# Kernel tuning notes

Hardware: AMD Instinct MI355X
Metric: run time of the kernel (lower is better)

Reference implementation:

```python
import jax, jax.numpy as jnp
import numpy as np

B, S, D = 64, 2048, 512

def setup_inputs() -> dict:
    key = jax.random.key(0)
    k1, k2, k3, k4, k5, k6 = jax.random.split(key, 6)
    hidden2 = jax.random.normal(k1, (B, D), dtype=jnp.float32)
    enc_key = jax.random.normal(k2, (B, S, D), dtype=jnp.float32)
    enc_value = jax.random.normal(k3, (B, S, D), dtype=jnp.float32)
    seq_lens = jax.random.randint(k4, (B,), 1, S + 1)  # valid lengths in [1, S]
    W = jax.random.normal(k5, (D, D), dtype=jnp.float32) / np.sqrt(D)
    b = jax.random.normal(k6, (D,), dtype=jnp.float32) * 0.01
    return {"hidden2": hidden2, "key": enc_key, "value": enc_value,
            "seq_lens": seq_lens, "W": W, "b": b}

def reference(hidden2, key, value, seq_lens, W, b):
    # query = Linear(hidden2): [B, D]
    query = hidden2 @ W.T + b
    # scores E = bmm(key, query): [B, S]
    E = jnp.einsum('bsd,bd->bs', key, query)
    # per-sample padding mask: positions >= seq_lens[i] get -inf
    mask = jnp.arange(S)[None, :] < seq_lens[:, None]  # [B, S]
    E = jnp.where(mask, E, -jnp.inf)
    attn = jax.nn.softmax(E, axis=-1)  # [B, S]
    context = jnp.einsum('bs,bsd->bd', attn, value)  # [B, D]
    return (context, attn[:, None, :])  # attn reshaped to [B, 1, S] as in torch
```

## Files before the change

### kernel.cpp

```cpp
#include <hip/hip_runtime.h>
#include <math.h>

#define BB 64
#define SS 2048
#define DD 512
#define SC 64
#define NC (SS / SC)

__global__ void query_kernel(const float* __restrict__ hidden2,
                             const float* __restrict__ W,
                             const float* __restrict__ bias,
                             float* __restrict__ q) {
    const int b    = blockIdx.y;
    const int wave = threadIdx.x >> 6;
    const int lane = threadIdx.x & 63;
    const int d    = blockIdx.x * 4 + wave;

    const float4* h4 = reinterpret_cast<const float4*>(hidden2 + (size_t)b * DD);
    const float4* w4 = reinterpret_cast<const float4*>(W + (size_t)d * DD);
    float4 a0 = h4[lane];
    float4 a1 = h4[64 + lane];
    float4 b0 = w4[lane];
    float4 b1 = w4[64 + lane];
    float p = a0.x*b0.x + a0.y*b0.y + a0.z*b0.z + a0.w*b0.w
            + a1.x*b1.x + a1.y*b1.y + a1.z*b1.z + a1.w*b1.w;
    #pragma unroll
    for (int off = 32; off; off >>= 1) p += __shfl_xor(p, off, 64);
    if (lane == 0) q[b * DD + d] = p + bias[d];
}

__global__ void chunk_kernel(const float* __restrict__ key,
                             const float* __restrict__ value,
                             const float* __restrict__ q,
                             const int* __restrict__ seq_lens,
                             float* __restrict__ attn,
                             float* __restrict__ mc,
                             float* __restrict__ lc,
                             float* __restrict__ ctxp) {
    const int b     = blockIdx.y;
    const int chunk = blockIdx.x;
    const int len   = seq_lens[b];
    const int s0    = chunk * SC;
    if (s0 >= len) return;
    const int nv = min(SC, len - s0);

    const int t    = threadIdx.x;
    const int wave = t >> 6;
    const int lane = t & 63;

    __shared__ float E_lds[SC];
    __shared__ float p_lds[SC];
    __shared__ float red[256];
    __shared__ float4 cred[128];

    const float4* q4 = reinterpret_cast<const float4*>(q + (size_t)b * DD);
    const float4 q0 = q4[lane];
    const float4 q1 = q4[64 + lane];

    for (int r = wave; r < nv; r += 4) {
        const float4* k4 =
            reinterpret_cast<const float4*>(key + ((size_t)b * SS + s0 + r) * DD);
        float4 k0 = k4[lane];
        float4 k1 = k4[64 + lane];
        float p = k0.x*q0.x + k0.y*q0.y + k0.z*q0.z + k0.w*q0.w
                + k1.x*q1.x + k1.y*q1.y + k1.z*q1.z + k1.w*q1.w;
        #pragma unroll
        for (int off = 32; off; off >>= 1) p += __shfl_xor(p, off, 64);
        if (lane == 0) E_lds[r] = p;
    }
    __syncthreads();

    red[t] = (t < nv) ? E_lds[t] : -INFINITY;
    __syncthreads();
    #pragma unroll
    for (int off = 128; off; off >>= 1) {
        if (t < off) red[t] = fmaxf(red[t], red[t + off]);
        __syncthreads();
    }
    const float m_c = red[0];
    __syncthreads();

    float pv = 0.f;
    if (t < nv) {
        pv = __expf(E_lds[t] - m_c);
        p_lds[t] = pv;
        attn[(size_t)b * SS + s0 + t] = pv;
    }
    red[t] = pv;
    __syncthreads();
    #pragma unroll
    for (int off = 128; off; off >>= 1) {
        if (t < off) red[t] += red[t + off];
        __syncthreads();
    }
    if (t == 0) {
        mc[b * NC + chunk] = m_c;
        lc[b * NC + chunk] = red[0];
    }

    const int d4   = t & 127;
    const int half = t >> 7;
    float4 acc = make_float4(0.f, 0.f, 0.f, 0.f);
    for (int r = half; r < nv; r += 2) {
        const float4 v = *reinterpret_cast<const float4*>(
            value + ((size_t)b * SS + s0 + r) * DD + 4 * d4);
        const float p = p_lds[r];
        acc.x += p * v.x; acc.y += p * v.y; acc.z += p * v.z; acc.w += p * v.w;
    }
    __syncthreads();
    if (half) cred[d4] = acc;
    __syncthreads();
    if (!half) {
        const float4 o = cred[d4];
        acc.x += o.x; acc.y += o.y; acc.z += o.z; acc.w += o.w;
        *reinterpret_cast<float4*>(ctxp + ((size_t)b * NC + chunk) * DD + 4 * d4) = acc;
    }
}

__global__ void combine_kernel(const float* __restrict__ mc,
                               const float* __restrict__ lc,
                               const float* __restrict__ ctxp,
                               const int* __restrict__ seq_lens,
                               float* __restrict__ attn,
                               float* __restrict__ ctx) {
    const int b   = blockIdx.x;
    const int t   = threadIdx.x;
    const int len = seq_lens[b];
    const int ncb = (len + SC - 1) / SC;

    __shared__ float sm[2];
    __shared__ float sa[NC];
    __shared__ float sc_[NC];

    if (t < 64) {
        const int lane = t;
        float m_c = (lane < ncb) ? mc[b * NC + lane] : -INFINITY;
        float l_c = (lane < ncb) ? lc[b * NC + lane] : 0.f;
        float m = m_c;
        #pragma unroll
        for (int off = 32; off; off >>= 1) m = fmaxf(m, __shfl_xor(m, off, 64));
        float le = l_c * __expf(m_c - m);
        float l = le;
        #pragma unroll
        for (int off = 32; off; off >>= 1) l += __shfl_xor(l, off, 64);
        if (lane == 0) { sm[0] = m; sm[1] = l; }
        if (lane < NC) {
            float e = (lane < ncb) ? __expf(m_c - m) : 0.f;
            sc_[lane] = e;
            sa[lane]  = e / l;
        }
    }
    __syncthreads();
    const float inv_l = 1.0f / sm[1];

    if (t < 128) {
        float4 acc = make_float4(0.f, 0.f, 0.f, 0.f);
        for (int c = 0; c < ncb; ++c) {
            const float4 v = *reinterpret_cast<const float4*>(
                ctxp + ((size_t)b * NC + c) * DD + 4 * t);
            const float s = sc_[c];
            acc.x += s * v.x; acc.y += s * v.y; acc.z += s * v.z; acc.w += s * v.w;
        }
        acc.x *= inv_l; acc.y *= inv_l; acc.z *= inv_l; acc.w *= inv_l;
        *reinterpret_cast<float4*>(ctx + (size_t)b * DD + 4 * t) = acc;
    }

    float* a = attn + (size_t)b * SS;
    for (int s = t; s < SS; s += 256) {
        if (s < len) a[s] *= sa[s >> 6];
        else         a[s]  = 0.f;
    }
}

extern "C" void kernel_launch(void* const* d_in, const int* in_sizes, int n_in,
                              void* d_out, int out_size, void* d_ws, size_t ws_size,
                              hipStream_t stream) {
    const float* hidden2  = (const float*)d_in[0];
    const float* key      = (const float*)d_in[1];
    const float* value    = (const float*)d_in[2];
    const int*   seq_lens = (const int*)  d_in[3];
    const float* W        = (const float*)d_in[4];
    const float* bias     = (const float*)d_in[5];

    float* out  = (float*)d_out;
    float* ctx  = out;
    float* attn = out + BB * DD;

    float* ws   = (float*)d_ws;
    float* q    = ws;
    float* mc   = ws + BB * DD;
    float* lc   = mc + BB * NC;
    float* ctxp = lc + BB * NC;

    query_kernel  <<<dim3(DD / 4, BB), 256, 0, stream>>>(hidden2, W, bias, q);
    chunk_kernel  <<<dim3(NC, BB),     256, 0, stream>>>(key, value, q, seq_lens,
                                                         attn, mc, lc, ctxp);
    combine_kernel<<<BB,               256, 0, stream>>>(mc, lc, ctxp, seq_lens,
                                                         attn, ctx);
}
```

Baseline: 491.5 us.

## Halve chunk size and replace LDS tree reductions with wave shuffles

Chunk size drops from 64 to 32 rows, doubling the number of chunk blocks to raise parallelism across the GPU. The block-wide max/sum reductions through shared memory with many barriers become a single-wave shuffle reduction, which is possible because a chunk now fits in one wave. The combine kernel is adjusted for 64 chunks per batch. In exchange, the partial context buffer and the combine work double, and each block does less work to amortize its launch cost.

Result: no change. 491.2 us (-0.1%).

```diff
diff --git a/kernel.cpp b/kernel.cpp
--- a/kernel.cpp
+++ b/kernel.cpp
@@ -4,7 +4,7 @@
 #define BB 64
 #define SS 2048
 #define DD 512
-#define SC 64
+#define SC 32
 #define NC (SS / SC)
 
 __global__ void query_kernel(const float* __restrict__ hidden2,
@@ -48,9 +48,8 @@
     const int wave = t >> 6;
     const int lane = t & 63;
 
-    __shared__ float E_lds[SC];
-    __shared__ float p_lds[SC];
-    __shared__ float red[256];
+    __shared__ float  E_lds[SC];
+    __shared__ float  p_lds[SC];
     __shared__ float4 cred[128];
 
     const float4* q4 = reinterpret_cast<const float4*>(q + (size_t)b * DD);
@@ -70,33 +69,22 @@
     }
     __syncthreads();
 
-    red[t] = (t < nv) ? E_lds[t] : -INFINITY;
+    if (wave == 0) {
+        const float e = (lane < nv) ? E_lds[lane] : -INFINITY;
+        float m = e;
+        #pragma unroll
+        for (int off = 32; off; off >>= 1) m = fmaxf(m, __shfl_xor(m, off, 64));
+        const float p = (lane < nv) ? __expf(e - m) : 0.f;
+        if (lane < nv) {
+            p_lds[lane] = p;
+            attn[(size_t)b * SS + s0 + lane] = p;
+        }
+        float l = p;
+        #pragma unroll
+        for (int off = 32; off; off >>= 1) l += __shfl_xor(l, off, 64);
+        if (lane == 0) { mc[b * NC + chunk] = m; lc[b * NC + chunk] = l; }
+    }
     __syncthreads();
-    #pragma unroll
-    for (int off = 128; off; off >>= 1) {
-        if (t < off) red[t] = fmaxf(red[t], red[t + off]);
-        __syncthreads();
-    }
-    const float m_c = red[0];
-    __syncthreads();
-
-    float pv = 0.f;
-    if (t < nv) {
-        pv = __expf(E_lds[t] - m_c);
-        p_lds[t] = pv;
-        attn[(size_t)b * SS + s0 + t] = pv;
-    }
-    red[t] = pv;
-    __syncthreads();
-    #pragma unroll
-    for (int off = 128; off; off >>= 1) {
-        if (t < off) red[t] += red[t + off];
-        __syncthreads();
-    }
-    if (t == 0) {
-        mc[b * NC + chunk] = m_c;
-        lc[b * NC + chunk] = red[0];
-    }
 
     const int d4   = t & 127;
     const int half = t >> 7;
@@ -128,30 +116,26 @@
     const int len = seq_lens[b];
     const int ncb = (len + SC - 1) / SC;
 
-    __shared__ float sm[2];
+    __shared__ float sm;
     __shared__ float sa[NC];
     __shared__ float sc_[NC];
 
     if (t < 64) {
-        const int lane = t;
-        float m_c = (lane < ncb) ? mc[b * NC + lane] : -INFINITY;
-        float l_c = (lane < ncb) ? lc[b * NC + lane] : 0.f;
+        const float m_c = (t < ncb) ? mc[b * NC + t] : -INFINITY;
+        const float l_c = (t < ncb) ? lc[b * NC + t] : 0.f;
         float m = m_c;
         #pragma unroll
         for (int off = 32; off; off >>= 1) m = fmaxf(m, __shfl_xor(m, off, 64));
-        float le = l_c * __expf(m_c - m);
-        float l = le;
+        float l = l_c * ((t < ncb) ? __expf(m_c - m) : 0.f);
         #pragma unroll
         for (int off = 32; off; off >>= 1) l += __shfl_xor(l, off, 64);
-        if (lane == 0) { sm[0] = m; sm[1] = l; }
-        if (lane < NC) {
-            float e = (lane < ncb) ? __expf(m_c - m) : 0.f;
-            sc_[lane] = e;
-            sa[lane]  = e / l;
-        }
+        const float e = (t < ncb) ? __expf(m_c - m) : 0.f;
+        sc_[t] = e;
+        sa[t]  = e / l;
+        if (t == 0) sm = l;
     }
     __syncthreads();
-    const float inv_l = 1.0f / sm[1];
+    const float inv_l = 1.0f / sm;
 
     if (t < 128) {
         float4 acc = make_float4(0.f, 0.f, 0.f, 0.f);
@@ -167,7 +151,7 @@
 
     float* a = attn + (size_t)b * SS;
     for (int s = t; s < SS; s += 256) {
-        if (s < len) a[s] *= sa[s >> 6];
+        if (s < len) a[s] *= sa[s >> 5];
         else         a[s]  = 0.f;
     }
 }
```
